# Optimization experiments

Measured on AMD Instinct MI355X. Metric: run time of the kernel, lower is better.

Reference implementation:

```python
import jax, jax.numpy as jnp
import numpy as np

B, E, N, F, D = 4, 8192, 1024, 512, 512
ALPHA = 0.2
NEG = -1e9  # keras Softmax large-negative masking constant


def setup_inputs() -> dict:
    key = jax.random.key(0)
    k_nodes, k_src, k_dst, k_w, k_a = jax.random.split(key, 5)
    nodes = jax.random.normal(k_nodes, (B, N, F), dtype=jnp.float32)
    src = jax.random.randint(k_src, (B, E), 0, N)
    dst = jax.random.randint(k_dst, (B, E), 0, N)
    Cmat = jax.nn.one_hot(src, N, dtype=jnp.float32)  # [B,E,N] source incidence
    Nmat = jax.nn.one_hot(dst, N, dtype=jnp.float32)  # [B,E,N] target incidence
    mask = jnp.ones((B, N, N), dtype=bool)  # present in input tuple but unused by call()
    w = jax.random.normal(k_w, (F, D), dtype=jnp.float32) * 0.05
    attention = jax.random.normal(k_a, (2 * D, 1), dtype=jnp.float32) * 0.05
    return {"nodes": nodes, "Cmat": Cmat, "Nmat": Nmat, "mask": mask,
            "w": w, "attention": attention}


def reference(nodes, Cmat, Nmat, mask, w, attention):
    z = jnp.matmul(nodes, w)                       # [B,N,D]
    z1 = jnp.matmul(Cmat, z)                       # [B,E,D] source embeddings
    z2 = jnp.matmul(Nmat, z)                       # [B,E,D] target embeddings
    couple = jnp.concatenate([z1, z2], axis=-1)    # [B,E,2D]
    att = jax.nn.leaky_relu(jnp.matmul(couple, attention), ALPHA)  # [B,E,1]
    att_t = jnp.swapaxes(att, -1, -2)              # [B,1,E]
    Cmat_t = jnp.swapaxes(Cmat, -1, -2)            # [B,N,E]
    scores = jnp.matmul(Cmat_t * att_t, Nmat)      # [B,N,N] per-edge score scattered
    adj = jnp.matmul(Cmat_t, Nmat)                 # [B,N,N] adjacency
    # keras Softmax(mask=adj): logits += (1 - cast(adj)) * NEG, softmax over last axis
    logits = scores + (1.0 - adj) * (-NEG) * -1.0 if False else scores + (1.0 - adj) * NEG
    adj_norm = jax.nn.softmax(logits, axis=-1) * adj
    out = jax.nn.leaky_relu(jnp.matmul(adj_norm, z), ALPHA)  # [B,N,D]
    return out
```

## Files before the change

### kernel.cpp

```cpp
#include <hip/hip_runtime.h>
#include <hip/hip_bf16.h>
#include <math.h>

#define BB 4
#define EE 8192
#define NN 1024
#define FF 512
#define DD 512
#define ALPHA 0.2f
#define SLOTS 64

typedef __attribute__((ext_vector_type(8))) short short8;
typedef __attribute__((ext_vector_type(4))) float f32x4;

static __device__ __forceinline__ float leaky(float x) { return x > 0.f ? x : ALPHA * x; }

static __device__ __forceinline__ float wave_sum(float v) {
#pragma unroll
    for (int m = 32; m >= 1; m >>= 1) v += __shfl_xor(v, m);
    return v;
}
static __device__ __forceinline__ float wave_max(float v) {
#pragma unroll
    for (int m = 32; m >= 1; m >>= 1) v = fmaxf(v, __shfl_xor(v, m));
    return v;
}
static __device__ __forceinline__ float dot4(float4 a, float4 b) {
    return a.x * b.x + a.y * b.y + a.z * b.z + a.w * b.w;
}

__global__ __launch_bounds__(256) void k_prep(const float* __restrict__ nodes,
                                              const float* __restrict__ w,
                                              const float* __restrict__ attn,
                                              __hip_bfloat16* __restrict__ Abf,
                                              __hip_bfloat16* __restrict__ BT,
                                              float* __restrict__ wa1, float* __restrict__ wa2,
                                              int* __restrict__ cur) {
    int bx = blockIdx.x;
    if (bx < 1024) {
        int idx = (bx * 256 + threadIdx.x) * 8;
        float4 v0 = *(const float4*)(nodes + idx);
        float4 v1 = *(const float4*)(nodes + idx + 4);
        __hip_bfloat16 tmp[8];
        tmp[0] = __float2bfloat16(v0.x); tmp[1] = __float2bfloat16(v0.y);
        tmp[2] = __float2bfloat16(v0.z); tmp[3] = __float2bfloat16(v0.w);
        tmp[4] = __float2bfloat16(v1.x); tmp[5] = __float2bfloat16(v1.y);
        tmp[6] = __float2bfloat16(v1.z); tmp[7] = __float2bfloat16(v1.w);
        *(short8*)(Abf + idx) = *(short8*)tmp;
        return;
    }
    if (bx < 1088) {
        __shared__ float tile[64][65];
        int tb = bx - 1024;
        int tk = tb >> 3, tn = tb & 7;
        int k0 = tk * 64, n0 = tn * 64;
#pragma unroll
        for (int it = 0; it < 16; ++it) {
            int id = it * 256 + threadIdx.x;
            int r = id >> 6, c = id & 63;
            tile[r][c] = w[(size_t)(k0 + r) * DD + n0 + c];
        }
        __syncthreads();
#pragma unroll
        for (int it = 0; it < 16; ++it) {
            int id = it * 256 + threadIdx.x;
            int r = id >> 6, c = id & 63;
            BT[(size_t)(n0 + r) * FF + k0 + c] = __float2bfloat16(tile[c][r]);
        }
        return;
    }
    if (bx < 1216) {
        int f = (bx - 1088) * 4 + (threadIdx.x >> 6);
        int lane = threadIdx.x & 63;
        const float4* wr = (const float4*)(w + (size_t)f * DD);
        const float4* a1p = (const float4*)attn;
        const float4* a2p = (const float4*)(attn + DD);
        float4 wv0 = wr[lane], wv1 = wr[64 + lane];
        float s1 = dot4(wv0, a1p[lane]) + dot4(wv1, a1p[64 + lane]);
        float s2 = dot4(wv0, a2p[lane]) + dot4(wv1, a2p[64 + lane]);
        s1 = wave_sum(s1);
        s2 = wave_sum(s2);
        if (lane == 0) {
            wa1[f] = s1;
            wa2[f] = s2;
        }
        return;
    }
    int4* cp = (int4*)cur;
    int4 z4 = {0, 0, 0, 0};
#pragma unroll
    for (int j = 0; j < 4; j++) cp[threadIdx.x * 4 + j] = z4;
}

#define BM 128
#define BN 64
#define BK 32
__global__ __launch_bounds__(256) void k_mega(const __hip_bfloat16* __restrict__ Abf,
                                              const __hip_bfloat16* __restrict__ BTbf,
                                              const float* __restrict__ nodes,
                                              const float* __restrict__ wa1,
                                              const float* __restrict__ wa2,
                                              const float* __restrict__ C,
                                              const float* __restrict__ Nm,
                                              float* __restrict__ Z,
                                              float* __restrict__ p1, float* __restrict__ p2,
                                              int* __restrict__ cur, int* __restrict__ sDst) {
    __shared__ short As[BM][BK + 8];
    __shared__ short Bs[BN][BK + 8];
    int bx = blockIdx.x;
    int t = threadIdx.x;
    int lane = t & 63;
    if (bx < 256) {
        int m0 = (bx & 31) * BM;
        int n0 = (bx >> 5) * BN;
        int wid = t >> 6;
        int wm = wid & 1, wn = wid >> 1;
        f32x4 acc[4][2] = {};
        const short* Ag = (const short*)Abf;
        const short* Bg = (const short*)BTbf;
        for (int k0 = 0; k0 < FF; k0 += BK) {
#pragma unroll
            for (int s = 0; s < 2; s++) {
                int cid = t + s * 256;
                int r = cid >> 2, cc = cid & 3;
                *(short8*)&As[r][cc * 8] = *(const short8*)&Ag[(size_t)(m0 + r) * FF + k0 + cc * 8];
            }
            {
                int r = t >> 2, cc = t & 3;
                *(short8*)&Bs[r][cc * 8] = *(const short8*)&Bg[(size_t)(n0 + r) * FF + k0 + cc * 8];
            }
            __syncthreads();
            short8 af[4];
            short8 bf[2];
#pragma unroll
            for (int m = 0; m < 4; m++)
                af[m] = *(const short8*)&As[wm * 64 + m * 16 + (lane & 15)][(lane >> 4) * 8];
#pragma unroll
            for (int n = 0; n < 2; n++)
                bf[n] = *(const short8*)&Bs[wn * 32 + n * 16 + (lane & 15)][(lane >> 4) * 8];
#pragma unroll
            for (int m = 0; m < 4; m++)
#pragma unroll
                for (int n = 0; n < 2; n++)
                    acc[m][n] = __builtin_amdgcn_mfma_f32_16x16x32_bf16(af[m], bf[n], acc[m][n], 0, 0, 0);
            __syncthreads();
        }
#pragma unroll
        for (int m = 0; m < 4; m++)
#pragma unroll
            for (int n = 0; n < 2; n++)
#pragma unroll
                for (int r = 0; r < 4; r++) {
                    int row = m0 + wm * 64 + m * 16 + (lane >> 4) * 4 + r;
                    int col = n0 + wn * 32 + n * 16 + (lane & 15);
                    Z[(size_t)row * DD + col] = acc[m][n][r];
                }
        return;
    }
    if (bx < 1280) {
        int rid = (bx - 256) * 4 + (t >> 6);
        const float4* nr = (const float4*)(nodes + (size_t)rid * FF);
        const float4* w1p = (const float4*)wa1;
        const float4* w2p = (const float4*)wa2;
        float4 v0 = nr[lane], v1 = nr[64 + lane];
        float s1 = dot4(v0, w1p[lane]) + dot4(v1, w1p[64 + lane]);
        float s2 = dot4(v0, w2p[lane]) + dot4(v1, w2p[64 + lane]);
        s1 = wave_sum(s1);
        s2 = wave_sum(s2);
        if (lane == 0) {
            p1[rid] = s1;
            p2[rid] = s2;
        }
        return;
    }
    int widx = (bx - 1280) * 4 + (t >> 6);
    const uint4* rc = (const uint4*)(C + (size_t)widx * NN);
    const uint4* rn = (const uint4*)(Nm + (size_t)widx * NN);
    int s = -1, d = -1;
#pragma unroll 1
    for (int c = 0; c < 4; ++c) {
        uint4 v, n;
        bool needS = (s < 0), needD = (d < 0);
        if (needS) v = rc[c * 64 + lane];
        if (needD) n = rn[c * 64 + lane];
        if (needS) {
            unsigned nz = v.x | v.y | v.z | v.w;
            unsigned long long m = __ballot(nz != 0u);
            if (m) {
                int idx = (c * 64 + lane) * 4 + (v.x ? 0 : (v.y ? 1 : (v.z ? 2 : 3)));
                s = __shfl(idx, (int)__ffsll(m) - 1);
            }
        }
        if (needD) {
            unsigned nz = n.x | n.y | n.z | n.w;
            unsigned long long m = __ballot(nz != 0u);
            if (m) {
                int idx = (c * 64 + lane) * 4 + (n.x ? 0 : (n.y ? 1 : (n.z ? 2 : 3)));
                d = __shfl(idx, (int)__ffsll(m) - 1);
            }
        }
        if (s >= 0 && d >= 0) break;
    }
    if (lane == 0) {
        int b = widx >> 13;
        int row = b * NN + s;
        int pos = atomicAdd(&cur[row], 1);
        if (pos < SLOTS) sDst[row * SLOTS + pos] = d;
    }
}

__global__ __launch_bounds__(256) void k_out(const int* __restrict__ cur,
                                             const int* __restrict__ sDst,
                                             const float* __restrict__ p1,
                                             const float* __restrict__ p2,
                                             const float* __restrict__ Z,
                                             float* __restrict__ out) {
    int rid = (blockIdx.x * 256 + threadIdx.x) >> 6;
    int lane = threadIdx.x & 63;
    if (rid >= BB * NN) return;
    int K = cur[rid];
    K = K > SLOTS ? SLOTS : K;
    int base = rid * SLOTS;
    int b = rid >> 10;
    f32x4 acc0 = {0.f, 0.f, 0.f, 0.f}, acc1 = {0.f, 0.f, 0.f, 0.f};
    f32x4* op = (f32x4*)(out + (size_t)rid * DD);
    if (K == 0) {
        op[lane] = acc0;
        op[64 + lane] = acc1;
        return;
    }
    float p1row = p1[rid];
    int de = (lane < K) ? sDst[base + lane] : -1;
    float ae = (lane < K) ? leaky(p1row + p2[(b << 10) + de]) : 0.f;
    float S = 0.f;
    int c = 0, firstk = 64;
    for (int k = 0; k < K; k++) {
        int dk = __shfl(de, k);
        float ak = __shfl(ae, k);
        bool mt = (lane < K) && (dk == de);
        if (mt) {
            S += ak;
            c++;
            if (k < firstk) firstk = k;
        }
    }
    float logit = (lane < K) ? (S + (float)(c - 1) * 1e9f) : -INFINITY;
    float M = wave_max(logit);
    float contrib = (lane < K && firstk == lane) ? __expf(logit - M) : 0.f;
    float Dsum = wave_sum(contrib);
    float wgt = (lane < K) ? __expf(logit - M) / Dsum : 0.f;
    for (int k = 0; k < K; k++) {
        int dj = __shfl(de, k);
        float wk = __shfl(wgt, k);
        const f32x4* zr = (const f32x4*)(Z + ((size_t)(b << 10) + dj) * DD);
        acc0 += wk * zr[lane];
        acc1 += wk * zr[64 + lane];
    }
    f32x4 o0, o1;
#pragma unroll
    for (int j = 0; j < 4; j++) {
        o0[j] = leaky(acc0[j]);
        o1[j] = leaky(acc1[j]);
    }
    op[lane] = o0;
    op[64 + lane] = o1;
}

extern "C" void kernel_launch(void* const* d_in, const int* in_sizes, int n_in,
                              void* d_out, int out_size, void* d_ws, size_t ws_size,
                              hipStream_t stream) {
    const float* nodes = (const float*)d_in[0];
    const float* Cmat = (const float*)d_in[1];
    const float* Nmat = (const float*)d_in[2];
    const float* w = (const float*)d_in[4];
    const float* attn = (const float*)d_in[5];
    float* out = (float*)d_out;

    char* ws = (char*)d_ws;
    size_t off = 0;
    auto alloc = [&](size_t bytes) -> void* {
        void* p = ws + off;
        off += (bytes + 255) & ~(size_t)255;
        return p;
    };
    float* Z = (float*)alloc((size_t)BB * NN * DD * 4);
    __hip_bfloat16* Abf = (__hip_bfloat16*)alloc((size_t)BB * NN * FF * 2);
    __hip_bfloat16* BT = (__hip_bfloat16*)alloc((size_t)FF * DD * 2);
    float* wa1 = (float*)alloc((size_t)FF * 4);
    float* wa2 = (float*)alloc((size_t)FF * 4);
    int* cur = (int*)alloc((size_t)BB * NN * 4);
    int* sDst = (int*)alloc((size_t)BB * NN * SLOTS * 4);
    float* p1 = (float*)alloc((size_t)BB * NN * 4);
    float* p2 = (float*)alloc((size_t)BB * NN * 4);

    k_prep<<<1217, 256, 0, stream>>>(nodes, w, attn, Abf, BT, wa1, wa2, cur);
    k_mega<<<1280 + 8192, 256, 0, stream>>>(Abf, BT, nodes, wa1, wa2, Cmat, Nmat,
                                            Z, p1, p2, cur, sDst);
    k_out<<<1024, 256, 0, stream>>>(cur, sDst, p1, p2, Z, out);
}
```

Baseline: 58.37 us.

## Fuse bf16 conversion of nodes into GEMM tile load and reorder mega-kernel blocks

```diff
diff --git a/kernel.cpp b/kernel.cpp
--- a/kernel.cpp
+++ b/kernel.cpp
@@ -28,31 +28,24 @@
 static __device__ __forceinline__ float dot4(float4 a, float4 b) {
     return a.x * b.x + a.y * b.y + a.z * b.z + a.w * b.w;
 }
-
-__global__ __launch_bounds__(256) void k_prep(const float* __restrict__ nodes,
-                                              const float* __restrict__ w,
+static __device__ __forceinline__ short8 cvt8(float4 a, float4 b) {
+    __hip_bfloat16 t[8];
+    t[0] = __float2bfloat16(a.x); t[1] = __float2bfloat16(a.y);
+    t[2] = __float2bfloat16(a.z); t[3] = __float2bfloat16(a.w);
+    t[4] = __float2bfloat16(b.x); t[5] = __float2bfloat16(b.y);
+    t[6] = __float2bfloat16(b.z); t[7] = __float2bfloat16(b.w);
+    return *(short8*)t;
+}
+
+__global__ __launch_bounds__(256) void k_prep(const float* __restrict__ w,
                                               const float* __restrict__ attn,
-                                              __hip_bfloat16* __restrict__ Abf,
                                               __hip_bfloat16* __restrict__ BT,
                                               float* __restrict__ wa1, float* __restrict__ wa2,
                                               int* __restrict__ cur) {
     int bx = blockIdx.x;
-    if (bx < 1024) {
-        int idx = (bx * 256 + threadIdx.x) * 8;
-        float4 v0 = *(const float4*)(nodes + idx);
-        float4 v1 = *(const float4*)(nodes + idx + 4);
-        __hip_bfloat16 tmp[8];
-        tmp[0] = __float2bfloat16(v0.x); tmp[1] = __float2bfloat16(v0.y);
-        tmp[2] = __float2bfloat16(v0.z); tmp[3] = __float2bfloat16(v0.w);
-        tmp[4] = __float2bfloat16(v1.x); tmp[5] = __float2bfloat16(v1.y);
-        tmp[6] = __float2bfloat16(v1.z); tmp[7] = __float2bfloat16(v1.w);
-        *(short8*)(Abf + idx) = *(short8*)tmp;
-        return;
-    }
-    if (bx < 1088) {
+    if (bx < 64) {
         __shared__ float tile[64][65];
-        int tb = bx - 1024;
-        int tk = tb >> 3, tn = tb & 7;
+        int tk = bx >> 3, tn = bx & 7;
         int k0 = tk * 64, n0 = tn * 64;
 #pragma unroll
         for (int it = 0; it < 16; ++it) {
@@ -69,8 +62,8 @@
         }
         return;
     }
-    if (bx < 1216) {
-        int f = (bx - 1088) * 4 + (threadIdx.x >> 6);
+    if (bx < 192) {
+        int f = (bx - 64) * 4 + (threadIdx.x >> 6);
         int lane = threadIdx.x & 63;
         const float4* wr = (const float4*)(w + (size_t)f * DD);
         const float4* a1p = (const float4*)attn;
@@ -95,9 +88,9 @@
 #define BM 128
 #define BN 64
 #define BK 32
-__global__ __launch_bounds__(256) void k_mega(const __hip_bfloat16* __restrict__ Abf,
+#define NEX 8192
+__global__ __launch_bounds__(256) void k_mega(const float* __restrict__ nodes,
                                               const __hip_bfloat16* __restrict__ BTbf,
-                                              const float* __restrict__ nodes,
                                               const float* __restrict__ wa1,
                                               const float* __restrict__ wa2,
                                               const float* __restrict__ C,
@@ -116,14 +109,15 @@
         int wid = t >> 6;
         int wm = wid & 1, wn = wid >> 1;
         f32x4 acc[4][2] = {};
-        const short* Ag = (const short*)Abf;
         const short* Bg = (const short*)BTbf;
         for (int k0 = 0; k0 < FF; k0 += BK) {
 #pragma unroll
             for (int s = 0; s < 2; s++) {
                 int cid = t + s * 256;
                 int r = cid >> 2, cc = cid & 3;
-                *(short8*)&As[r][cc * 8] = *(const short8*)&Ag[(size_t)(m0 + r) * FF + k0 + cc * 8];
+                const float4* ap = (const float4*)&nodes[(size_t)(m0 + r) * FF + k0 + cc * 8];
+                As[r][0] = As[r][0];
+                *(short8*)&As[r][cc * 8] = cvt8(ap[0], ap[1]);
             }
             {
                 int r = t >> 2, cc = t & 3;
@@ -157,55 +151,55 @@
                 }
         return;
     }
-    if (bx < 1280) {
-        int rid = (bx - 256) * 4 + (t >> 6);
-        const float4* nr = (const float4*)(nodes + (size_t)rid * FF);
-        const float4* w1p = (const float4*)wa1;
-        const float4* w2p = (const float4*)wa2;
-        float4 v0 = nr[lane], v1 = nr[64 + lane];
-        float s1 = dot4(v0, w1p[lane]) + dot4(v1, w1p[64 + lane]);
-        float s2 = dot4(v0, w2p[lane]) + dot4(v1, w2p[64 + lane]);
-        s1 = wave_sum(s1);
-        s2 = wave_sum(s2);
+    if (bx < 256 + NEX) {
+        int widx = (bx - 256) * 4 + (t >> 6);
+        const uint4* rc = (const uint4*)(C + (size_t)widx * NN);
+        const uint4* rn = (const uint4*)(Nm + (size_t)widx * NN);
+        int s = -1, d = -1;
+#pragma unroll 1
+        for (int c = 0; c < 4; ++c) {
+            uint4 v, n;
+            bool needS = (s < 0), needD = (d < 0);
+            if (needS) v = rc[c * 64 + lane];
+            if (needD) n = rn[c * 64 + lane];
+            if (needS) {
+                unsigned nz = v.x | v.y | v.z | v.w;
+                unsigned long long m = __ballot(nz != 0u);
+                if (m) {
+                    int idx = (c * 64 + lane) * 4 + (v.x ? 0 : (v.y ? 1 : (v.z ? 2 : 3)));
+                    s = __shfl(idx, (int)__ffsll(m) - 1);
+                }
+            }
+            if (needD) {
+                unsigned nz = n.x | n.y | n.z | n.w;
+                unsigned long long m = __ballot(nz != 0u);
+                if (m) {
+                    int idx = (c * 64 + lane) * 4 + (n.x ? 0 : (n.y ? 1 : (n.z ? 2 : 3)));
+                    d = __shfl(idx, (int)__ffsll(m) - 1);
+                }
+            }
+            if (s >= 0 && d >= 0) break;
+        }
         if (lane == 0) {
-            p1[rid] = s1;
-            p2[rid] = s2;
-        }
-        return;
-    }
-    int widx = (bx - 1280) * 4 + (t >> 6);
-    const uint4* rc = (const uint4*)(C + (size_t)widx * NN);
-    const uint4* rn = (const uint4*)(Nm + (size_t)widx * NN);
-    int s = -1, d = -1;
-#pragma unroll 1
-    for (int c = 0; c < 4; ++c) {
-        uint4 v, n;
-        bool needS = (s < 0), needD = (d < 0);
-        if (needS) v = rc[c * 64 + lane];
-        if (needD) n = rn[c * 64 + lane];
-        if (needS) {
-            unsigned nz = v.x | v.y | v.z | v.w;
-            unsigned long long m = __ballot(nz != 0u);
-            if (m) {
-                int idx = (c * 64 + lane) * 4 + (v.x ? 0 : (v.y ? 1 : (v.z ? 2 : 3)));
-                s = __shfl(idx, (int)__ffsll(m) - 1);
-            }
-        }
-        if (needD) {
-            unsigned nz = n.x | n.y | n.z | n.w;
-            unsigned long long m = __ballot(nz != 0u);
-            if (m) {
-                int idx = (c * 64 + lane) * 4 + (n.x ? 0 : (n.y ? 1 : (n.z ? 2 : 3)));
-                d = __shfl(idx, (int)__ffsll(m) - 1);
-            }
-        }
-        if (s >= 0 && d >= 0) break;
-    }
+            int b = widx >> 13;
+            int row = b * NN + s;
+            int pos = atomicAdd(&cur[row], 1);
+            if (pos < SLOTS) sDst[row * SLOTS + pos] = d;
+        }
+        return;
+    }
+    int rid = (bx - 256 - NEX) * 4 + (t >> 6);
+    const float4* nr = (const float4*)(nodes + (size_t)rid * FF);
+    const float4* w1p = (const float4*)wa1;
+    const float4* w2p = (const float4*)wa2;
+    float4 v0 = nr[lane], v1 = nr[64 + lane];
+    float s1 = dot4(v0, w1p[lane]) + dot4(v1, w1p[64 + lane]);
+    float s2 = dot4(v0, w2p[lane]) + dot4(v1, w2p[64 + lane]);
+    s1 = wave_sum(s1);
+    s2 = wave_sum(s2);
     if (lane == 0) {
-        int b = widx >> 13;
-        int row = b * NN + s;
-        int pos = atomicAdd(&cur[row], 1);
-        if (pos < SLOTS) sDst[row * SLOTS + pos] = d;
+        p1[rid] = s1;
+        p2[rid] = s2;
     }
 }
 
@@ -249,10 +243,20 @@
     float contrib = (lane < K && firstk == lane) ? __expf(logit - M) : 0.f;
     float Dsum = wave_sum(contrib);
     float wgt = (lane < K) ? __expf(logit - M) / Dsum : 0.f;
-    for (int k = 0; k < K; k++) {
+    const float* Zb = Z + ((size_t)(b << 10)) * DD;
+#pragma unroll
+    for (int k = 0; k < 16; k++) {
+        bool pr = (k < K);
+        int dj = pr ? __shfl(de, k) : 0;
+        float wk = pr ? __shfl(wgt, k) : 0.f;
+        const f32x4* zr = (const f32x4*)(Zb + (size_t)dj * DD);
+        acc0 += wk * zr[lane];
+        acc1 += wk * zr[64 + lane];
+    }
+    for (int k = 16; k < K; k++) {
         int dj = __shfl(de, k);
         float wk = __shfl(wgt, k);
-        const f32x4* zr = (const f32x4*)(Z + ((size_t)(b << 10) + dj) * DD);
+        const f32x4* zr = (const f32x4*)(Zb + (size_t)dj * DD);
         acc0 += wk * zr[lane];
         acc1 += wk * zr[64 + lane];
     }
@@ -284,7 +288,6 @@
         return p;
     };
     float* Z = (float*)alloc((size_t)BB * NN * DD * 4);
-    __hip_bfloat16* Abf = (__hip_bfloat16*)alloc((size_t)BB * NN * FF * 2);
     __hip_bfloat16* BT = (__hip_bfloat16*)alloc((size_t)FF * DD * 2);
     float* wa1 = (float*)alloc((size_t)FF * 4);
     float* wa2 = (float*)alloc((size_t)FF * 4);
@@ -293,8 +296,8 @@
     float* p1 = (float*)alloc((size_t)BB * NN * 4);
     float* p2 = (float*)alloc((size_t)BB * NN * 4);
 
-    k_prep<<<1217, 256, 0, stream>>>(nodes, w, attn, Abf, BT, wa1, wa2, cur);
-    k_mega<<<1280 + 8192, 256, 0, stream>>>(Abf, BT, nodes, wa1, wa2, Cmat, Nmat,
-                                            Z, p1, p2, cur, sDst);
+    k_prep<<<193, 256, 0, stream>>>(w, attn, BT, wa1, wa2, cur);
+    k_mega<<<256 + NEX + 1024, 256, 0, stream>>>(nodes, BT, wa1, wa2, Cmat, Nmat,
+                                                 Z, p1, p2, cur, sDst);
     k_out<<<1024, 256, 0, stream>>>(cur, sDst, p1, p2, Z, out);
 }
```

Result: faster. 53.70 us (-8.0%).
